# Kernel tuning notes

Hardware: AMD Instinct MI355X
Metric: run time of the kernel (lower is better)

## Reference

```python
import jax, jax.numpy as jnp
import numpy as np

B, L, F = 64, 200, 64  # batch, max_route_len, link+route features

def setup_inputs() -> dict:
    key = jax.random.key(0)
    k1, k2 = jax.random.split(key)
    inp = jax.random.normal(k1, (B, L, L, F), dtype=jnp.float32)
    theta = jax.random.normal(k2, (L, L, F), dtype=jnp.float32)
    return {"input": inp, "theta": theta}

def reference(input, theta):
    # output[b,i,j] = input[b,i,j] . theta[i,j]  == per-position dot product
    return jnp.einsum('bijf,ijf->bij', input, theta)
```

## Files before the change

kernel.cpp:

```cpp
#include <hip/hip_runtime.h>


#define BQ 64
#define LQ 200
#define FQ 64
#define IJ (LQ * LQ)
#define EPB 16
#define CHUNKS (IJ / EPB)

__global__ __launch_bounds__(256)
void IRLLinearModel_42786464203479_kernel(const float* __restrict__ inp,
                                          const float* __restrict__ theta,
                                          float* __restrict__ out) {
    const int chunk = blockIdx.x / BQ;
    const int b     = blockIdx.x % BQ;

    const int g = threadIdx.x >> 4;
    const int s = threadIdx.x & 15;

    const int ij = chunk * EPB + g;

    const size_t in_off = ((size_t)b * IJ + ij) * FQ + (size_t)s * 4;
    const size_t th_off = (size_t)ij * FQ + (size_t)s * 4;

    const float4 a = *reinterpret_cast<const float4*>(inp + in_off);
    const float4 t = *reinterpret_cast<const float4*>(theta + th_off);

    float p = a.x * t.x + a.y * t.y + a.z * t.z + a.w * t.w;

    p += __shfl_xor(p, 1);
    p += __shfl_xor(p, 2);
    p += __shfl_xor(p, 4);
    p += __shfl_xor(p, 8);

    if (s == 0) {
        out[(size_t)b * IJ + ij] = p;
    }
}

extern "C" void kernel_launch(void* const* d_in, const int* in_sizes, int n_in,
                              void* d_out, int out_size, void* d_ws, size_t ws_size,
                              hipStream_t stream) {
    const float* inp   = (const float*)d_in[0];
    const float* theta = (const float*)d_in[1];
    float* out = (float*)d_out;

    const int grid = CHUNKS * BQ;
    IRLLinearModel_42786464203479_kernel<<<grid, 256, 0, stream>>>(inp, theta, out);
}
```

Measured before the change: 156.1 us.

## Loop over batch per block to reuse theta, with nontemporal streaming loads

Each block now handles one 16-position chunk across all 64 batch entries. Theta is loaded once into registers and reused, instead of being reloaded by every batch block. Input loads and output stores use nontemporal hints, and four batch entries are processed per unrolled step for more memory-level parallelism. The grid shrinks by a factor of 64 to 2500 blocks, which may reduce latency hiding and occupancy on a memory-bound kernel.

```diff
diff --git a/kernel.cpp b/kernel.cpp
--- a/kernel.cpp
+++ b/kernel.cpp
@@ -8,33 +8,57 @@
 #define EPB 16
 #define CHUNKS (IJ / EPB)
 
+typedef float f32x4 __attribute__((ext_vector_type(4)));
+
 __global__ __launch_bounds__(256)
 void IRLLinearModel_42786464203479_kernel(const float* __restrict__ inp,
                                           const float* __restrict__ theta,
                                           float* __restrict__ out) {
-    const int chunk = blockIdx.x / BQ;
-    const int b     = blockIdx.x % BQ;
+    const int chunk = blockIdx.x;
 
     const int g = threadIdx.x >> 4;
     const int s = threadIdx.x & 15;
 
     const int ij = chunk * EPB + g;
 
-    const size_t in_off = ((size_t)b * IJ + ij) * FQ + (size_t)s * 4;
-    const size_t th_off = (size_t)ij * FQ + (size_t)s * 4;
+    const f32x4 t = *reinterpret_cast<const f32x4*>(theta + (size_t)ij * FQ + (size_t)s * 4);
 
-    const float4 a = *reinterpret_cast<const float4*>(inp + in_off);
-    const float4 t = *reinterpret_cast<const float4*>(theta + th_off);
+    const float* in_base = inp + (size_t)ij * FQ + (size_t)s * 4;
+    const size_t bstride = (size_t)IJ * FQ;
 
-    float p = a.x * t.x + a.y * t.y + a.z * t.z + a.w * t.w;
+    float* out_base = out + ij;
 
-    p += __shfl_xor(p, 1);
-    p += __shfl_xor(p, 2);
-    p += __shfl_xor(p, 4);
-    p += __shfl_xor(p, 8);
+    #pragma unroll
+    for (int b0 = 0; b0 < BQ; b0 += 4) {
+        const f32x4 a0 = __builtin_nontemporal_load(
+            reinterpret_cast<const f32x4*>(in_base + (size_t)(b0 + 0) * bstride));
+        const f32x4 a1 = __builtin_nontemporal_load(
+            reinterpret_cast<const f32x4*>(in_base + (size_t)(b0 + 1) * bstride));
+        const f32x4 a2 = __builtin_nontemporal_load(
+            reinterpret_cast<const f32x4*>(in_base + (size_t)(b0 + 2) * bstride));
+        const f32x4 a3 = __builtin_nontemporal_load(
+            reinterpret_cast<const f32x4*>(in_base + (size_t)(b0 + 3) * bstride));
 
-    if (s == 0) {
-        out[(size_t)b * IJ + ij] = p;
+        float p0 = a0.x * t.x + a0.y * t.y + a0.z * t.z + a0.w * t.w;
+        float p1 = a1.x * t.x + a1.y * t.y + a1.z * t.z + a1.w * t.w;
+        float p2 = a2.x * t.x + a2.y * t.y + a2.z * t.z + a2.w * t.w;
+        float p3 = a3.x * t.x + a3.y * t.y + a3.z * t.z + a3.w * t.w;
+
+        p0 += __shfl_xor(p0, 1);  p1 += __shfl_xor(p1, 1);
+        p2 += __shfl_xor(p2, 1);  p3 += __shfl_xor(p3, 1);
+        p0 += __shfl_xor(p0, 2);  p1 += __shfl_xor(p1, 2);
+        p2 += __shfl_xor(p2, 2);  p3 += __shfl_xor(p3, 2);
+        p0 += __shfl_xor(p0, 4);  p1 += __shfl_xor(p1, 4);
+        p2 += __shfl_xor(p2, 4);  p3 += __shfl_xor(p3, 4);
+        p0 += __shfl_xor(p0, 8);  p1 += __shfl_xor(p1, 8);
+        p2 += __shfl_xor(p2, 8);  p3 += __shfl_xor(p3, 8);
+
+        if (s == 0) {
+            __builtin_nontemporal_store(p0, out_base + (size_t)(b0 + 0) * IJ);
+            __builtin_nontemporal_store(p1, out_base + (size_t)(b0 + 1) * IJ);
+            __builtin_nontemporal_store(p2, out_base + (size_t)(b0 + 2) * IJ);
+            __builtin_nontemporal_store(p3, out_base + (size_t)(b0 + 3) * IJ);
+        }
     }
 }
 
@@ -45,6 +69,5 @@
     const float* theta = (const float*)d_in[1];
     float* out = (float*)d_out;
 
-    const int grid = CHUNKS * BQ;
-    IRLLinearModel_42786464203479_kernel<<<grid, 256, 0, stream>>>(inp, theta, out);
+    IRLLinearModel_42786464203479_kernel<<<CHUNKS, 256, 0, stream>>>(inp, theta, out);
 }
```

After: 135.3 us. -13.3%, faster.
